# Optimization experiments

Measured on AMD Instinct MI355X. Metric: run time of the kernel, lower is better.

## Reference

```python
import jax, jax.numpy as jnp
import numpy as np

D_MODEL = 640
KW = 32                                  # kernel_width -> content_kernel (compression (1,1))
SUPER = np.array([5, 5, 2, 1, 1])        # supersampling per subhead
DIL = np.array([1, 1, 2, 4, 8])          # dilation rate per subhead
SUBHEADS = 5
HEADS = int(SUPER.sum())                 # 14
DH = D_MODEL // SUBHEADS                 # 128
B, N = 2, 1024
KC = KW                                  # content kernel width
DIL_PER_HEAD = np.repeat(DIL, SUPER)     # dilation used by each of the 14 value heads


def _windows(seq, bias, dil):
    """Banded (dilated, stride-1, 'same'-padded) windows of a projected sequence.

    seq: (B, N, DH). The original zero-pads the raw sequence, then applies the
    per-head Linear; projecting a zero vector yields the bias, so padding the
    projected sequence with `bias` is mathematically identical.
    Returns (B, N, KC, DH) with out[b, l, j] = padded[b, l + j*dil].
    """
    dil = int(dil)
    pad_total = (KC - 1) * dil           # effective kernel minus 1, stride 1 -> same length
    pl = pad_total // 2
    pr = pad_total - pl
    b = seq.shape[0]
    left = jnp.broadcast_to(bias, (b, pl, DH))
    right = jnp.broadcast_to(bias, (b, pr, DH))
    padded = jnp.concatenate([left, seq, right], axis=1)
    idx = jnp.arange(N)[:, None] + jnp.arange(KC)[None, :] * dil  # (N, KC)
    return padded[:, idx]


def setup_inputs() -> dict:
    key = jax.random.key(0)
    ks = jax.random.split(key, 13)
    f = lambda k, sh, s=1.0: jax.random.normal(k, sh, dtype=jnp.float32) * s
    return {
        "query": f(ks[0], (B, N, D_MODEL)),
        "key": f(ks[1], (B, N, D_MODEL)),
        "value": f(ks[2], (B, N, D_MODEL)),
        "Qk": f(ks[3], (SUBHEADS, DH, D_MODEL), 0.04),
        "Qb": f(ks[4], (SUBHEADS, DH), 0.02),
        "Kk": f(ks[5], (SUBHEADS, DH, D_MODEL), 0.04),
        "Kb": f(ks[6], (SUBHEADS, DH), 0.02),
        "Vk": f(ks[7], (HEADS, DH, D_MODEL), 0.04),
        "Vb": f(ks[8], (HEADS, DH), 0.02),
        "Sk": f(ks[9], (HEADS, KC, KC), 0.1),   # Pos_Sampling kernel, Kq=1 so in=out=KC
        "Sb": f(ks[10], (HEADS, KC), 0.02),
        "Ck": f(ks[11], (D_MODEL, HEADS * DH), 0.02),  # Collapse kernel
        "Cb": f(ks[12], (D_MODEL,), 0.0),
    }


def reference(query, key, value, Qk, Qb, Kk, Kb, Vk, Vb, Sk, Sb, Ck, Cb):
    # Per-subhead Q/K projections (query_kernel=1, stride=1 -> one query per position)
    q = jnp.einsum('bnd,sod->bnso', query, Qk) + Qb          # (B,N,5,DH)
    kproj = jnp.einsum('bnd,sod->bnso', key, Kk) + Kb        # (B,N,5,DH)
    kwin = jnp.stack(
        [_windows(kproj[:, :, s], Kb[s], DIL[s]) for s in range(SUBHEADS)],
        axis=2)                                              # (B,N,5,KC,DH)
    # Banded scores (original applies no 1/sqrt(d) scaling)
    score = jnp.einsum('bnsd,bnskd->bnsk', q, kwin)          # (B,N,5,KC)
    # Supersample subhead scores into heads, then learned positional resampling
    score = jnp.repeat(score, SUPER, axis=2, total_repeat_length=HEADS)  # (B,N,14,KC)
    score = jnp.einsum('bnhk,hjk->bnhj', score, Sk) + Sb     # Pos_Sampling Linear
    w = jax.nn.softmax(score, axis=-1)
    # Per-head value projection; each head windows with its subhead's dilation
    vproj = jnp.einsum('bnd,hod->bnho', value, Vk) + Vb      # (B,N,14,DH)
    vwin = jnp.stack(
        [_windows(vproj[:, :, h], Vb[h], DIL_PER_HEAD[h]) for h in range(HEADS)],
        axis=2)                                              # (B,N,14,KC,DH)
    attn = jnp.einsum('bnhk,bnhkd->bnhd', w, vwin)           # (B,N,14,DH)
    flat = attn.reshape(attn.shape[0], attn.shape[1], HEADS * DH)
    return jnp.einsum('bnf,of->bno', flat, Ck) + Cb          # (B,N,D_MODEL)
```

## Files before the change

kernel.cpp:

```cpp
#include <hip/hip_runtime.h>
#include <hip/hip_bf16.h>

using bf16 = __hip_bfloat16;
typedef __attribute__((ext_vector_type(8))) short s16x8;
typedef __attribute__((ext_vector_type(4))) short s16x4;
typedef __attribute__((ext_vector_type(4))) float f32x4;
typedef unsigned int u32;

__device__ __forceinline__ float b2f(short u) {
    union { float f; u32 i; } x; x.i = ((u32)(unsigned short)u) << 16; return x.f;
}
__device__ __forceinline__ short f2b(float f) {
    bf16 h = (bf16)f; return *(short*)&h;
}

struct CvtArgs { const float* src[10]; bf16* dst[10]; int n[10]; int bb[11]; };
__global__ __launch_bounds__(256)
void convert_kernel(CvtArgs a) {
    const int blk = blockIdx.x;
    int s = 0;
    while (s < 9 && blk >= a.bb[s + 1]) ++s;
    const int base = (blk - a.bb[s]) * 1024 + threadIdx.x * 4;
    if (base >= a.n[s]) return;
    float4 v = *(const float4*)(a.src[s] + base);
    ushort4 o;
    o.x = (unsigned short)f2b(v.x); o.y = (unsigned short)f2b(v.y);
    o.z = (unsigned short)f2b(v.z); o.w = (unsigned short)f2b(v.w);
    *(ushort4*)(a.dst[s] + base) = o;
}

template<int BM, int BN, bool A_F32, bool OUT_F32>
__device__ __forceinline__ void gemm_pipe(
    const void* __restrict__ A, const bf16* __restrict__ W,
    const bf16* __restrict__ bias, void* __restrict__ out,
    int m0, int n0, int N, int K, bf16* lA, bf16* lB) {
    constexpr int WM = BM / 2, WN = BN / 2, FM = WM / 16, FN = WN / 16;
    constexpr int SA = BM / 64, SB = BN / 64;
    const int tid = threadIdx.x;
    const int wave = tid >> 6, lane = tid & 63;
    const int wr = wave >> 1, wc = wave & 1;
    const int quad = lane >> 4, lm = lane & 15;
    uint4 ra[SA], rb[SB];

    auto loadA = [&](int k0) {
#pragma unroll
        for (int q = 0; q < SA; ++q) {
            const int sl = q * 256 + tid, row = sl >> 2, col = (sl & 3) * 8;
            if (A_F32) {
                const float* g = (const float*)A + (size_t)(m0 + row) * K + k0 + col;
                float4 f0 = *(const float4*)g;
                float4 f1 = *(const float4*)(g + 4);
                union { uint4 u; short h[8]; } p;
                p.h[0] = f2b(f0.x); p.h[1] = f2b(f0.y); p.h[2] = f2b(f0.z); p.h[3] = f2b(f0.w);
                p.h[4] = f2b(f1.x); p.h[5] = f2b(f1.y); p.h[6] = f2b(f1.z); p.h[7] = f2b(f1.w);
                ra[q] = p.u;
            } else {
                ra[q] = *(const uint4*)((const bf16*)A + (size_t)(m0 + row) * K + k0 + col);
            }
        }
    };
    auto loadB = [&](int k0) {
#pragma unroll
        for (int q = 0; q < SB; ++q) {
            const int sl = q * 256 + tid, row = sl >> 2, col = (sl & 3) * 8;
            rb[q] = *(const uint4*)(W + (size_t)(n0 + row) * K + k0 + col);
        }
    };

    f32x4 acc[FM][FN] = {};
    loadA(0); loadB(0);
    for (int k0 = 0; k0 < K; k0 += 32) {
#pragma unroll
        for (int q = 0; q < SA; ++q) *(uint4*)(lA + (q * 256 + tid) * 8) = ra[q];
#pragma unroll
        for (int q = 0; q < SB; ++q) *(uint4*)(lB + (q * 256 + tid) * 8) = rb[q];
        __syncthreads();
        if (k0 + 32 < K) { loadA(k0 + 32); loadB(k0 + 32); }
        s16x8 af[FM], bf_[FN];
#pragma unroll
        for (int i = 0; i < FM; ++i)
            af[i] = *(const s16x8*)&lA[(wr * WM + i * 16 + lm) * 32 + quad * 8];
#pragma unroll
        for (int j = 0; j < FN; ++j)
            bf_[j] = *(const s16x8*)&lB[(wc * WN + j * 16 + lm) * 32 + quad * 8];
#pragma unroll
        for (int i = 0; i < FM; ++i)
#pragma unroll
            for (int j = 0; j < FN; ++j)
                acc[i][j] = __builtin_amdgcn_mfma_f32_16x16x32_bf16(af[i], bf_[j], acc[i][j], 0, 0, 0);
        __syncthreads();
    }
#pragma unroll
    for (int i = 0; i < FM; ++i) {
        const int rbase = m0 + wr * WM + i * 16 + quad * 4;
#pragma unroll
        for (int j = 0; j < FN; ++j) {
            const int col = n0 + wc * WN + j * 16 + lm;
            const float bv = (float)bias[col];
#pragma unroll
            for (int r = 0; r < 4; ++r) {
                float v = acc[i][j][r] + bv;
                size_t off = (size_t)(rbase + r) * N + col;
                if (OUT_F32) ((float*)out)[off] = v;
                else         ((bf16*)out)[off] = (bf16)v;
            }
        }
    }
}

__global__ __launch_bounds__(256)
void proj_kernel(const float* __restrict__ q, const float* __restrict__ k,
                 const float* __restrict__ v,
                 const bf16* __restrict__ Qkc, const bf16* __restrict__ Kkc,
                 const bf16* __restrict__ Vkc,
                 const bf16* __restrict__ Qbc, const bf16* __restrict__ Kbc,
                 const bf16* __restrict__ Vbc,
                 bf16* __restrict__ qp, bf16* __restrict__ kp,
                 bf16* __restrict__ vp) {
    __shared__ __align__(16) bf16 lA[128 * 32];
    __shared__ __align__(16) bf16 lB[64 * 32];
    const int L = blockIdx.x, xcd = L & 7, i = L >> 3;
    const int m0 = (xcd * 2 + i / 48) * 128;
    const int nid = i % 48;
    if (nid < 10)
        gemm_pipe<128, 64, true, false>(q, Qkc, Qbc, qp, m0, nid * 64, 640, 640, lA, lB);
    else if (nid < 20)
        gemm_pipe<128, 64, true, false>(k, Kkc, Kbc, kp, m0, (nid - 10) * 64, 640, 640, lA, lB);
    else
        gemm_pipe<128, 64, true, false>(v, Vkc, Vbc, vp, m0, (nid - 20) * 64, 1792, 640, lA, lB);
}

__global__ __launch_bounds__(256)
void collapse_kernel(const bf16* __restrict__ atn, const bf16* __restrict__ Ckc,
                     const bf16* __restrict__ Cbc, float* __restrict__ out) {
    __shared__ __align__(16) bf16 lA[64 * 32];
    __shared__ __align__(16) bf16 lB[64 * 32];
    const int L = blockIdx.x, xcd = L & 7, i = L >> 3;
    const int m0 = (xcd * 4 + i / 10) * 64;
    const int n0 = (i % 10) * 64;
    gemm_pipe<64, 64, false, true>(atn, Ckc, Cbc, out, m0, n0, 640, 1792, lA, lB);
}

__global__ __launch_bounds__(256)
void attn_v6(const bf16* __restrict__ qp, const bf16* __restrict__ kp,
             const bf16* __restrict__ vp,
             const bf16* __restrict__ Kbc, const bf16* __restrict__ Vbc,
             const bf16* __restrict__ Skc, const bf16* __restrict__ Sbc,
             bf16* __restrict__ atn) {
    const int pos = ((blockIdx.x & 7) << 8) | (blockIdx.x >> 3);
    const int b = pos >> 10, l = pos & 1023;
    const int t = threadIdx.x;
    __shared__ float qs[640];
    __shared__ float sc5[5 * 32];
    __shared__ float sc14[14 * 32];
    __shared__ float w14T[32 * 14];

    if (t < 80) {
        s16x8 qv = *(const s16x8*)((const short*)qp + (size_t)pos * 640 + t * 8);
#pragma unroll
        for (int r = 0; r < 8; ++r) qs[t * 8 + r] = b2f(qv[r]);
    }
    __syncthreads();

    {
        const int j = t >> 3, p = t & 7;
#pragma unroll
        for (int s = 0; s < 5; ++s) {
            const int dil = (s < 2) ? 1 : (1 << (s - 1));
            const int pl = (31 * dil) >> 1;
            const int row = l + j * dil - pl;
            const float* q = qs + s * 128 + p * 4;
            const short* kr = (row >= 0 && row < 1024)
                ? (const short*)kp + (size_t)((b << 10) | row) * 640 + s * 128 + p * 4
                : (const short*)Kbc + s * 128 + p * 4;
            float acc = 0.f;
#pragma unroll
            for (int g = 0; g < 4; ++g) {
                s16x4 kv = *(const s16x4*)(kr + g * 32);
                float4 qv = *(const float4*)(q + g * 32);
                acc += qv.x * b2f(kv[0]) + qv.y * b2f(kv[1])
                     + qv.z * b2f(kv[2]) + qv.w * b2f(kv[3]);
            }
            acc += __shfl_xor(acc, 1);
            acc += __shfl_xor(acc, 2);
            acc += __shfl_xor(acc, 4);
            if (p == 0) sc5[s * 32 + j] = acc;
        }
    }
    __syncthreads();

    for (int idx = t; idx < 448; idx += 256) {
        const int h = idx >> 5;
        const int s = (h < 5) ? 0 : (h < 10) ? 1 : (h < 12) ? 2 : (h == 12) ? 3 : 4;
        const s16x8* sk = (const s16x8*)((const short*)Skc + idx * 32);
        const float* sc = sc5 + s * 32;
        float acc = b2f(((const short*)Sbc)[idx]);
#pragma unroll
        for (int g = 0; g < 4; ++g) {
            s16x8 kk = sk[g];
#pragma unroll
            for (int r = 0; r < 8; ++r) acc += sc[g * 8 + r] * b2f(kk[r]);
        }
        sc14[idx] = acc;
    }
    __syncthreads();

    if (t < 224) {
        const int h = t >> 4, u = t & 15;
        float s0 = sc14[h * 32 + u], s1 = sc14[h * 32 + u + 16];
        float mx = fmaxf(s0, s1);
#pragma unroll
        for (int m = 1; m < 16; m <<= 1) mx = fmaxf(mx, __shfl_xor(mx, m));
        float e0 = __expf(s0 - mx), e1 = __expf(s1 - mx);
        float sum = e0 + e1;
#pragma unroll
        for (int m = 1; m < 16; m <<= 1) sum += __shfl_xor(sum, m);
        float inv = 1.f / sum;
        w14T[u * 14 + h] = e0 * inv;
        w14T[(u + 16) * 14 + h] = e1 * inv;
    }
    __syncthreads();

    if (t < 224) {
        const int h = t >> 4, d8 = (t & 15) * 8;
        const int dil = (h < 10) ? 1 : (h < 12) ? 2 : (h == 12) ? 4 : 8;
        const int pl = (31 * dil) >> 1;
        const int col = h * 128 + d8;
        float acc[8] = {};
#pragma unroll
        for (int j = 0; j < 32; ++j) {
            const int row = l + j * dil - pl;
            const short* src = (row >= 0 && row < 1024)
                ? (const short*)vp + (size_t)((b << 10) | row) * 1792 + col
                : (const short*)Vbc + col;
            s16x8 v8 = *(const s16x8*)src;
            const float w = w14T[j * 14 + h];
#pragma unroll
            for (int r = 0; r < 8; ++r) acc[r] += w * b2f(v8[r]);
        }
        union { uint4 u; short h16[8]; } o;
#pragma unroll
        for (int r = 0; r < 8; ++r) o.h16[r] = f2b(acc[r]);
        *(uint4*)((short*)atn + (size_t)pos * 1792 + col) = o.u;
    }
}

extern "C" void kernel_launch(void* const* d_in, const int* in_sizes, int n_in,
                              void* d_out, int out_size, void* d_ws, size_t ws_size,
                              hipStream_t stream) {
    const int M = 2048;
    char* w = (char*)d_ws;
    size_t off = 0;
    auto alloc = [&](size_t bytes) -> char* {
        off = (off + 255) & ~(size_t)255;
        char* p = w + off; off += bytes; return p;
    };
    bf16* Qkc = (bf16*)alloc(409600 * 2);
    bf16* Qbc = (bf16*)alloc(640 * 2);
    bf16* Kkc = (bf16*)alloc(409600 * 2);
    bf16* Kbc = (bf16*)alloc(640 * 2);
    bf16* Vkc = (bf16*)alloc(1146880 * 2);
    bf16* Vbc = (bf16*)alloc(1792 * 2);
    bf16* Skc = (bf16*)alloc(14336 * 2);
    bf16* Sbc = (bf16*)alloc(448 * 2);
    bf16* Ckc = (bf16*)alloc(1146880 * 2);
    bf16* Cbc = (bf16*)alloc(640 * 2);
    bf16* qp = (bf16*)alloc((size_t)M * 640 * 2);
    bf16* kp = (bf16*)alloc((size_t)M * 640 * 2);
    bf16* vp = (bf16*)alloc((size_t)M * 1792 * 2);
    bf16* atn = (bf16*)alloc((size_t)M * 1792 * 2);

    CvtArgs ca;
    bf16* dsts[10] = {Qkc, Qbc, Kkc, Kbc, Vkc, Vbc, Skc, Sbc, Ckc, Cbc};
    const int ns[10] = {409600, 640, 409600, 640, 1146880, 1792, 14336, 448, 1146880, 640};
    int cum = 0;
    for (int i = 0; i < 10; ++i) {
        ca.src[i] = (const float*)d_in[3 + i];
        ca.dst[i] = dsts[i];
        ca.n[i] = ns[i];
        ca.bb[i] = cum;
        cum += (ns[i] + 1023) / 1024;
    }
    ca.bb[10] = cum;

    dim3 blk(256);
    convert_kernel<<<dim3(cum), blk, 0, stream>>>(ca);
    proj_kernel<<<dim3(768), blk, 0, stream>>>(
        (const float*)d_in[0], (const float*)d_in[1], (const float*)d_in[2],
        Qkc, Kkc, Vkc, Qbc, Kbc, Vbc, qp, kp, vp);
    attn_v6<<<dim3(2048), blk, 0, stream>>>(qp, kp, vp, Kbc, Vbc, Skc, Sbc, atn);
    collapse_kernel<<<dim3(320), blk, 0, stream>>>(atn, Ckc, Cbc, (float*)d_out);
}
```

Measured before the change: 167.5 us.

## Split-K the collapse GEMM with atomic adds and widen key loads in attention

```diff
diff --git a/kernel.cpp b/kernel.cpp
--- a/kernel.cpp
+++ b/kernel.cpp
@@ -29,11 +29,11 @@
     *(ushort4*)(a.dst[s] + base) = o;
 }
 
-template<int BM, int BN, bool A_F32, bool OUT_F32>
+template<int BM, int BN, bool A_F32, bool OUT_F32, bool ATOMIC>
 __device__ __forceinline__ void gemm_pipe(
     const void* __restrict__ A, const bf16* __restrict__ W,
     const bf16* __restrict__ bias, void* __restrict__ out,
-    int m0, int n0, int N, int K, bf16* lA, bf16* lB) {
+    int m0, int n0, int N, int K, int kbeg, int kend, bf16* lA, bf16* lB) {
     constexpr int WM = BM / 2, WN = BN / 2, FM = WM / 16, FN = WN / 16;
     constexpr int SA = BM / 64, SB = BN / 64;
     const int tid = threadIdx.x;
@@ -68,14 +68,14 @@
     };
 
     f32x4 acc[FM][FN] = {};
-    loadA(0); loadB(0);
-    for (int k0 = 0; k0 < K; k0 += 32) {
+    loadA(kbeg); loadB(kbeg);
+    for (int k0 = kbeg; k0 < kend; k0 += 32) {
 #pragma unroll
         for (int q = 0; q < SA; ++q) *(uint4*)(lA + (q * 256 + tid) * 8) = ra[q];
 #pragma unroll
         for (int q = 0; q < SB; ++q) *(uint4*)(lB + (q * 256 + tid) * 8) = rb[q];
         __syncthreads();
-        if (k0 + 32 < K) { loadA(k0 + 32); loadB(k0 + 32); }
+        if (k0 + 32 < kend) { loadA(k0 + 32); loadB(k0 + 32); }
         s16x8 af[FM], bf_[FN];
 #pragma unroll
         for (int i = 0; i < FM; ++i)
@@ -96,13 +96,14 @@
 #pragma unroll
         for (int j = 0; j < FN; ++j) {
             const int col = n0 + wc * WN + j * 16 + lm;
-            const float bv = (float)bias[col];
+            const float bv = bias ? (float)bias[col] : 0.f;
 #pragma unroll
             for (int r = 0; r < 4; ++r) {
                 float v = acc[i][j][r] + bv;
                 size_t off = (size_t)(rbase + r) * N + col;
-                if (OUT_F32) ((float*)out)[off] = v;
-                else         ((bf16*)out)[off] = (bf16)v;
+                if (ATOMIC)       atomicAdd((float*)out + off, v);
+                else if (OUT_F32) ((float*)out)[off] = v;
+                else              ((bf16*)out)[off] = (bf16)v;
             }
         }
     }
@@ -123,11 +124,11 @@
     const int m0 = (xcd * 2 + i / 48) * 128;
     const int nid = i % 48;
     if (nid < 10)
-        gemm_pipe<128, 64, true, false>(q, Qkc, Qbc, qp, m0, nid * 64, 640, 640, lA, lB);
+        gemm_pipe<128, 64, true, false, false>(q, Qkc, Qbc, qp, m0, nid * 64, 640, 640, 0, 640, lA, lB);
     else if (nid < 20)
-        gemm_pipe<128, 64, true, false>(k, Kkc, Kbc, kp, m0, (nid - 10) * 64, 640, 640, lA, lB);
+        gemm_pipe<128, 64, true, false, false>(k, Kkc, Kbc, kp, m0, (nid - 10) * 64, 640, 640, 0, 640, lA, lB);
     else
-        gemm_pipe<128, 64, true, false>(v, Vkc, Vbc, vp, m0, (nid - 20) * 64, 1792, 640, lA, lB);
+        gemm_pipe<128, 64, true, false, false>(v, Vkc, Vbc, vp, m0, (nid - 20) * 64, 1792, 640, 0, 640, lA, lB);
 }
 
 __global__ __launch_bounds__(256)
@@ -136,9 +137,12 @@
     __shared__ __align__(16) bf16 lA[64 * 32];
     __shared__ __align__(16) bf16 lB[64 * 32];
     const int L = blockIdx.x, xcd = L & 7, i = L >> 3;
-    const int m0 = (xcd * 4 + i / 10) * 64;
-    const int n0 = (i % 10) * 64;
-    gemm_pipe<64, 64, false, true>(atn, Ckc, Cbc, out, m0, n0, 640, 1792, lA, lB);
+    const int m0 = (xcd * 4 + i / 40) * 64;
+    const int rem = i % 40;
+    const int n0 = (rem >> 2) * 64;
+    const int ks = rem & 3;
+    gemm_pipe<64, 64, false, true, true>(atn, Ckc, ks ? nullptr : Cbc, out,
+        m0, n0, 640, 1792, ks * 448, ks * 448 + 448, lA, lB);
 }
 
 __global__ __launch_bounds__(256)
@@ -169,17 +173,20 @@
             const int dil = (s < 2) ? 1 : (1 << (s - 1));
             const int pl = (31 * dil) >> 1;
             const int row = l + j * dil - pl;
-            const float* q = qs + s * 128 + p * 4;
+            const float* q = qs + s * 128 + p * 8;
             const short* kr = (row >= 0 && row < 1024)
-                ? (const short*)kp + (size_t)((b << 10) | row) * 640 + s * 128 + p * 4
-                : (const short*)Kbc + s * 128 + p * 4;
+                ? (const short*)kp + (size_t)((b << 10) | row) * 640 + s * 128 + p * 8
+                : (const short*)Kbc + s * 128 + p * 8;
             float acc = 0.f;
 #pragma unroll
-            for (int g = 0; g < 4; ++g) {
-                s16x4 kv = *(const s16x4*)(kr + g * 32);
-                float4 qv = *(const float4*)(q + g * 32);
-                acc += qv.x * b2f(kv[0]) + qv.y * b2f(kv[1])
-                     + qv.z * b2f(kv[2]) + qv.w * b2f(kv[3]);
+            for (int g = 0; g < 2; ++g) {
+                s16x8 kv = *(const s16x8*)(kr + g * 64);
+                float4 q0 = *(const float4*)(q + g * 64);
+                float4 q1 = *(const float4*)(q + g * 64 + 4);
+                acc += q0.x * b2f(kv[0]) + q0.y * b2f(kv[1])
+                     + q0.z * b2f(kv[2]) + q0.w * b2f(kv[3])
+                     + q1.x * b2f(kv[4]) + q1.y * b2f(kv[5])
+                     + q1.z * b2f(kv[6]) + q1.w * b2f(kv[7]);
             }
             acc += __shfl_xor(acc, 1);
             acc += __shfl_xor(acc, 2);
@@ -270,6 +277,8 @@
     bf16* vp = (bf16*)alloc((size_t)M * 1792 * 2);
     bf16* atn = (bf16*)alloc((size_t)M * 1792 * 2);
 
+    hipMemsetAsync(d_out, 0, (size_t)out_size, stream);
+
     CvtArgs ca;
     bf16* dsts[10] = {Qkc, Qbc, Kkc, Kbc, Vkc, Vbc, Skc, Sbc, Ckc, Cbc};
     const int ns[10] = {409600, 640, 409600, 640, 1146880, 1792, 14336, 448, 1146880, 640};
@@ -289,5 +298,5 @@
         (const float*)d_in[0], (const float*)d_in[1], (const float*)d_in[2],
         Qkc, Kkc, Vkc, Qbc, Kbc, Vbc, qp, kp, vp);
     attn_v6<<<dim3(2048), blk, 0, stream>>>(qp, kp, vp, Kbc, Vbc, Skc, Sbc, atn);
-    collapse_kernel<<<dim3(320), blk, 0, stream>>>(atn, Ckc, Cbc, (float*)d_out);
-}
+    collapse_kernel<<<dim3(1280), blk, 0, stream>>>(atn, Ckc, Cbc, (float*)d_out);
+}
```

Result: slower. 172.1 us (+2.7%).

## Double-buffer GEMM LDS tiles with direct global-to-LDS loads; widen score key loads

Applied to the files above, without the earlier changes.

```diff
diff --git a/kernel.cpp b/kernel.cpp
--- a/kernel.cpp
+++ b/kernel.cpp
@@ -12,6 +12,12 @@
 }
 __device__ __forceinline__ short f2b(float f) {
     bf16 h = (bf16)f; return *(short*)&h;
+}
+
+__device__ __forceinline__ void g2l16(const void* g, void* l) {
+    __builtin_amdgcn_global_load_lds(
+        (const __attribute__((address_space(1))) void*)g,
+        (__attribute__((address_space(3))) void*)l, 16, 0, 0);
 }
 
 struct CvtArgs { const float* src[10]; bf16* dst[10]; int n[10]; int bb[11]; };
@@ -35,60 +41,79 @@
     const bf16* __restrict__ bias, void* __restrict__ out,
     int m0, int n0, int N, int K, bf16* lA, bf16* lB) {
     constexpr int WM = BM / 2, WN = BN / 2, FM = WM / 16, FN = WN / 16;
-    constexpr int SA = BM / 64, SB = BN / 64;
+    constexpr int SA = BM / 64;
+    constexpr int CA = BM / 64;
+    constexpr int CB = BN / 64;
+    constexpr int ASZ = BM * 32, BSZ = BN * 32;
     const int tid = threadIdx.x;
-    const int wave = tid >> 6, lane = tid & 63;
+    const int wave = tid >> 6;
+    const int lane = tid & 63;
     const int wr = wave >> 1, wc = wave & 1;
     const int quad = lane >> 4, lm = lane & 15;
-    uint4 ra[SA], rb[SB];
-
-    auto loadA = [&](int k0) {
+    uint4 ra[SA];
+
+    auto issueB = [&](int k0, int buf) {
+#pragma unroll
+        for (int c = 0; c < CB; ++c) {
+            const int sl = c * 256 + tid, row = sl >> 2, col = (sl & 3) * 8;
+            g2l16(W + (size_t)(n0 + row) * K + k0 + col,
+                  lB + buf * BSZ + (c * 256 + wave * 64) * 8);
+        }
+    };
+    auto issueA = [&](int k0, int buf) {
+#pragma unroll
+        for (int c = 0; c < CA; ++c) {
+            const int sl = c * 256 + tid, row = sl >> 2, col = (sl & 3) * 8;
+            g2l16((const bf16*)A + (size_t)(m0 + row) * K + k0 + col,
+                  lA + buf * ASZ + (c * 256 + wave * 64) * 8);
+        }
+    };
+    auto loadA_f32 = [&](int k0) {
 #pragma unroll
         for (int q = 0; q < SA; ++q) {
             const int sl = q * 256 + tid, row = sl >> 2, col = (sl & 3) * 8;
-            if (A_F32) {
-                const float* g = (const float*)A + (size_t)(m0 + row) * K + k0 + col;
-                float4 f0 = *(const float4*)g;
-                float4 f1 = *(const float4*)(g + 4);
-                union { uint4 u; short h[8]; } p;
-                p.h[0] = f2b(f0.x); p.h[1] = f2b(f0.y); p.h[2] = f2b(f0.z); p.h[3] = f2b(f0.w);
-                p.h[4] = f2b(f1.x); p.h[5] = f2b(f1.y); p.h[6] = f2b(f1.z); p.h[7] = f2b(f1.w);
-                ra[q] = p.u;
-            } else {
-                ra[q] = *(const uint4*)((const bf16*)A + (size_t)(m0 + row) * K + k0 + col);
-            }
-        }
-    };
-    auto loadB = [&](int k0) {
-#pragma unroll
-        for (int q = 0; q < SB; ++q) {
-            const int sl = q * 256 + tid, row = sl >> 2, col = (sl & 3) * 8;
-            rb[q] = *(const uint4*)(W + (size_t)(n0 + row) * K + k0 + col);
-        }
+            const float* g = (const float*)A + (size_t)(m0 + row) * K + k0 + col;
+            float4 f0 = *(const float4*)g;
+            float4 f1 = *(const float4*)(g + 4);
+            union { uint4 u; short h[8]; } p;
+            p.h[0] = f2b(f0.x); p.h[1] = f2b(f0.y); p.h[2] = f2b(f0.z); p.h[3] = f2b(f0.w);
+            p.h[4] = f2b(f1.x); p.h[5] = f2b(f1.y); p.h[6] = f2b(f1.z); p.h[7] = f2b(f1.w);
+            ra[q] = p.u;
+        }
+    };
+    auto writeA = [&](int buf) {
+#pragma unroll
+        for (int q = 0; q < SA; ++q)
+            *(uint4*)(lA + buf * ASZ + (q * 256 + tid) * 8) = ra[q];
     };
 
     f32x4 acc[FM][FN] = {};
-    loadA(0); loadB(0);
+    issueB(0, 0);
+    if (A_F32) { loadA_f32(0); writeA(0); } else { issueA(0, 0); }
+    __syncthreads();
+
+    int cur = 0;
     for (int k0 = 0; k0 < K; k0 += 32) {
-#pragma unroll
-        for (int q = 0; q < SA; ++q) *(uint4*)(lA + (q * 256 + tid) * 8) = ra[q];
-#pragma unroll
-        for (int q = 0; q < SB; ++q) *(uint4*)(lB + (q * 256 + tid) * 8) = rb[q];
-        __syncthreads();
-        if (k0 + 32 < K) { loadA(k0 + 32); loadB(k0 + 32); }
+        const bool more = (k0 + 32 < K);
+        if (more) {
+            issueB(k0 + 32, cur ^ 1);
+            if (A_F32) loadA_f32(k0 + 32); else issueA(k0 + 32, cur ^ 1);
+        }
         s16x8 af[FM], bf_[FN];
 #pragma unroll
         for (int i = 0; i < FM; ++i)
-            af[i] = *(const s16x8*)&lA[(wr * WM + i * 16 + lm) * 32 + quad * 8];
+            af[i] = *(const s16x8*)&lA[cur * ASZ + (wr * WM + i * 16 + lm) * 32 + quad * 8];
 #pragma unroll
         for (int j = 0; j < FN; ++j)
-            bf_[j] = *(const s16x8*)&lB[(wc * WN + j * 16 + lm) * 32 + quad * 8];
+            bf_[j] = *(const s16x8*)&lB[cur * BSZ + (wc * WN + j * 16 + lm) * 32 + quad * 8];
 #pragma unroll
         for (int i = 0; i < FM; ++i)
 #pragma unroll
             for (int j = 0; j < FN; ++j)
                 acc[i][j] = __builtin_amdgcn_mfma_f32_16x16x32_bf16(af[i], bf_[j], acc[i][j], 0, 0, 0);
+        if (more && A_F32) writeA(cur ^ 1);
         __syncthreads();
+        cur ^= 1;
     }
 #pragma unroll
     for (int i = 0; i < FM; ++i) {
@@ -117,8 +142,8 @@
                  const bf16* __restrict__ Vbc,
                  bf16* __restrict__ qp, bf16* __restrict__ kp,
                  bf16* __restrict__ vp) {
-    __shared__ __align__(16) bf16 lA[128 * 32];
-    __shared__ __align__(16) bf16 lB[64 * 32];
+    __shared__ __align__(16) bf16 lA[2 * 128 * 32];
+    __shared__ __align__(16) bf16 lB[2 * 64 * 32];
     const int L = blockIdx.x, xcd = L & 7, i = L >> 3;
     const int m0 = (xcd * 2 + i / 48) * 128;
     const int nid = i % 48;
@@ -133,8 +158,8 @@
 __global__ __launch_bounds__(256)
 void collapse_kernel(const bf16* __restrict__ atn, const bf16* __restrict__ Ckc,
                      const bf16* __restrict__ Cbc, float* __restrict__ out) {
-    __shared__ __align__(16) bf16 lA[64 * 32];
-    __shared__ __align__(16) bf16 lB[64 * 32];
+    __shared__ __align__(16) bf16 lA[2 * 64 * 32];
+    __shared__ __align__(16) bf16 lB[2 * 64 * 32];
     const int L = blockIdx.x, xcd = L & 7, i = L >> 3;
     const int m0 = (xcd * 4 + i / 10) * 64;
     const int n0 = (i % 10) * 64;
@@ -169,17 +194,20 @@
             const int dil = (s < 2) ? 1 : (1 << (s - 1));
             const int pl = (31 * dil) >> 1;
             const int row = l + j * dil - pl;
-            const float* q = qs + s * 128 + p * 4;
+            const float* q = qs + s * 128 + p * 8;
             const short* kr = (row >= 0 && row < 1024)
-                ? (const short*)kp + (size_t)((b << 10) | row) * 640 + s * 128 + p * 4
-                : (const short*)Kbc + s * 128 + p * 4;
+                ? (const short*)kp + (size_t)((b << 10) | row) * 640 + s * 128 + p * 8
+                : (const short*)Kbc + s * 128 + p * 8;
             float acc = 0.f;
 #pragma unroll
-            for (int g = 0; g < 4; ++g) {
-                s16x4 kv = *(const s16x4*)(kr + g * 32);
-                float4 qv = *(const float4*)(q + g * 32);
-                acc += qv.x * b2f(kv[0]) + qv.y * b2f(kv[1])
-                     + qv.z * b2f(kv[2]) + qv.w * b2f(kv[3]);
+            for (int g = 0; g < 2; ++g) {
+                s16x8 kv = *(const s16x8*)(kr + g * 64);
+                float4 q0 = *(const float4*)(q + g * 64);
+                float4 q1 = *(const float4*)(q + g * 64 + 4);
+                acc += q0.x * b2f(kv[0]) + q0.y * b2f(kv[1])
+                     + q0.z * b2f(kv[2]) + q0.w * b2f(kv[3])
+                     + q1.x * b2f(kv[4]) + q1.y * b2f(kv[5])
+                     + q1.z * b2f(kv[6]) + q1.w * b2f(kv[7]);
             }
             acc += __shfl_xor(acc, 1);
             acc += __shfl_xor(acc, 2);
```

Result: no change. 167.0 us, median of 3 (-0.3%).
